# Optimization experiments

Hardware: AMD Instinct MI355X
Metric: run time of the kernel (lower is better)

## Reference

```python
import jax, jax.numpy as jnp
import numpy as np
import math

FEAT_DIM = 128
N_BANK = 1000000
K_NEG = 4096
BATCH = 256
T = 0.5
MOMENTUM = 0.5
EPS = 1e-7


def setup_inputs() -> dict:
    key = jax.random.key(0)
    k1, k2, k3, k4, k5, k6 = jax.random.split(key, 6)
    stdv = 1.0 / math.sqrt(FEAT_DIM / 3)
    memory_l = jax.random.uniform(k1, (N_BANK, FEAT_DIM), minval=-stdv, maxval=stdv, dtype=jnp.float32)
    memory_ab = jax.random.uniform(k2, (N_BANK, FEAT_DIM), minval=-stdv, maxval=stdv, dtype=jnp.float32)
    l = jax.random.normal(k3, (BATCH, FEAT_DIM), dtype=jnp.float32)
    ab = jax.random.normal(k4, (BATCH, FEAT_DIM), dtype=jnp.float32)
    y = jax.random.randint(k5, (BATCH,), 0, N_BANK, dtype=jnp.int32)
    idx = jax.random.randint(k6, (BATCH, K_NEG + 1), 0, N_BANK, dtype=jnp.int32)
    idx = idx.at[:, 0].set(y)  # positive sample in slot 0, as in torch forward
    return {"l": l, "ab": ab, "memory_l": memory_l, "memory_ab": memory_ab, "y": y, "idx": idx}


def _l2_normalize(x):
    # matches torch: x / (sqrt(sum(x^2)) + eps)
    return x / (jnp.sqrt(jnp.sum(x * x, axis=1, keepdims=True)) + EPS)


def _momentum_update(memory, y, x_norm):
    # gather rows, momentum mix, renormalize, scatter back
    pos = memory[y] * MOMENTUM + x_norm * (1.0 - MOMENTUM)          # [B, D]
    norm = jnp.sqrt(jnp.sum(pos * pos, axis=1, keepdims=True))
    return memory.at[y].set(pos / norm)


def reference(l, ab, memory_l, memory_ab, y, idx):
    outputSize = memory_l.shape[0]
    ln = _l2_normalize(l)
    abn = _l2_normalize(ab)

    # gather negatives+positive from the AB bank, score against l features
    w_ab = jax.lax.stop_gradient(memory_ab[idx])                     # [B, K+1, D]
    P_l = jnp.exp(jnp.einsum('bkd,bd->bk', w_ab, ln) / T)[..., None]  # [B, K+1, 1]
    Z_l = jnp.mean(P_l) * outputSize
    out_l = P_l / Z_l

    w_l = jax.lax.stop_gradient(memory_l[idx])                       # [B, K+1, D]
    P_ab = jnp.exp(jnp.einsum('bkd,bd->bk', w_l, abn) / T)[..., None]
    Z_ab = jnp.mean(P_ab) * outputSize
    out_ab = P_ab / Z_ab

    # momentum scatter update of the memory banks (no_grad in torch)
    new_memory_l = jax.lax.stop_gradient(_momentum_update(memory_l, y, ln))
    new_memory_ab = jax.lax.stop_gradient(_momentum_update(memory_ab, y, abn))

    return out_l, out_ab, new_memory_l, new_memory_ab
```

## Files before the change

### kernel.cpp

```cpp
#include <hip/hip_runtime.h>
#include <math.h>
#include <stdint.h>

#define FEAT   128
#define NBANK  1000000
#define KP1    4097
#define BATCH  256
#define INV_T  2.0f
#define EPS_N  1e-7f

constexpr size_t TOTP   = (size_t)BATCH * KP1;
constexpr size_t O_OUTL = 0;
constexpr size_t O_OUTA = TOTP;
constexpr size_t O_MEML = 2 * TOTP;
constexpr size_t O_MEMA = O_MEML + (size_t)NBANK * FEAT;

constexpr int RPB   = 16;
constexpr int NBUCK = NBANK / RPB;
constexpr int CAP   = 128;

constexpr size_t WS_LN   = 0;
constexpr size_t WS_ABN  = 32768;
constexpr size_t WS_PL   = 65544;
constexpr size_t WS_PA   = 65800;
constexpr size_t WS_U32  = 66560;

typedef float vfloat4 __attribute__((ext_vector_type(4)));

__device__ __forceinline__ float dot4(vfloat4 a, vfloat4 b) {
    return a.x * b.x + a.y * b.y + a.z * b.z + a.w * b.w;
}

__global__ void norm_zero_kernel(const float* __restrict__ l,
                                 const float* __restrict__ ab,
                                 float* __restrict__ ws,
                                 unsigned int* __restrict__ cnt) {
    int b    = blockIdx.x;
    int lane = threadIdx.x;
    for (int i = b * 64 + lane; i < NBUCK; i += 512 * 64) cnt[i] = 0u;
    const float* src;
    float*       dst;
    if (b < BATCH) { src = l  + (size_t)b * FEAT;            dst = ws + WS_LN  + (size_t)b * FEAT; }
    else           { src = ab + (size_t)(b - BATCH) * FEAT;  dst = ws + WS_ABN + (size_t)(b - BATCH) * FEAT; }
    float2 v = *(const float2*)(src + 2 * lane);
    float  ss = v.x * v.x + v.y * v.y;
    #pragma unroll
    for (int m = 1; m < 64; m <<= 1) ss += __shfl_xor(ss, m, 64);
    float inv = 1.0f / (sqrtf(ss) + EPS_N);
    ((float2*)dst)[lane] = make_float2(v.x * inv, v.y * inv);
}

__global__ void build_kernel(const int* __restrict__ idx,
                             unsigned int* __restrict__ cnt,
                             unsigned int* __restrict__ ent) {
    size_t stride = (size_t)gridDim.x * blockDim.x;
    for (size_t p = (size_t)blockIdx.x * blockDim.x + threadIdx.x; p < TOTP; p += stride) {
        int row = idx[p];
        int b   = (int)(p / KP1);
        int k   = (int)(p - (size_t)b * KP1);
        int bucket = row >> 4;
        unsigned int pos = atomicAdd(&cnt[bucket], 1u);
        if (pos < (unsigned int)CAP)
            ent[(size_t)bucket * CAP + pos] =
                ((unsigned int)b << 17) | ((unsigned int)k << 4) | (unsigned int)(row & 15);
    }
}

__global__ __launch_bounds__(256) void copyscore_kernel(
        const float* __restrict__ src, float* __restrict__ dst,
        const float* __restrict__ qtab, float* __restrict__ pout,
        const unsigned int* __restrict__ cnt,
        const unsigned int* __restrict__ ent) {
    int blk = blockIdx.x;
    int tid = threadIdx.x;
    size_t fbase = (size_t)blk * RPB * FEAT;

    int c = min((int)cnt[blk], CAP);

    const vfloat4* s = (const vfloat4*)(src + fbase);
    vfloat4 v0 = s[tid], v1 = s[256 + tid];
    vfloat4* d = (vfloat4*)(dst + fbase);
    d[tid] = v0; d[256 + tid] = v1;

    int g = tid >> 4, lane16 = tid & 15;
    for (int i = g; i < c; i += 16) {
        unsigned int ev = ent[(size_t)blk * CAP + i];
        int rloc = (int)(ev & 15u);
        int k    = (int)((ev >> 4) & 0x1FFFu);
        int b    = (int)(ev >> 17);
        const vfloat4* rp = (const vfloat4*)(src + fbase + (size_t)rloc * FEAT) + lane16 * 2;
        vfloat4 w0 = rp[0], w1 = rp[1];
        const vfloat4* qp = (const vfloat4*)(qtab + (size_t)b * FEAT) + lane16 * 2;
        vfloat4 q0 = qp[0], q1 = qp[1];
        float dv = dot4(w0, q0) + dot4(w1, q1);
        #pragma unroll
        for (int m = 1; m < 16; m <<= 1) dv += __shfl_xor(dv, m, 64);
        if (lane16 == 0) pout[(size_t)b * KP1 + k] = __expf(dv * INV_T);
    }
}

__global__ void zsum_kernel(const float* __restrict__ out,
                            float* __restrict__ pl, float* __restrict__ pa) {
    __shared__ float sl[256], sa[256];
    int i = blockIdx.x, t = threadIdx.x;
    const float* bl = out + O_OUTL + (size_t)i * KP1;
    const float* ba = out + O_OUTA + (size_t)i * KP1;
    float a = 0.f, b = 0.f;
    for (int p = t; p < KP1; p += 256) { a += bl[p]; b += ba[p]; }
    sl[t] = a; sa[t] = b;
    __syncthreads();
    for (int s = 128; s > 0; s >>= 1) {
        if (t < s) { sl[t] += sl[t + s]; sa[t] += sa[t + s]; }
        __syncthreads();
    }
    if (t == 0) { pl[i] = sl[0]; pa[i] = sa[0]; }
}

__global__ void finish_kernel(const float* __restrict__ pl,
                              const float* __restrict__ pa,
                              const float* __restrict__ mem_l,
                              const float* __restrict__ mem_ab,
                              const int*   __restrict__ y,
                              const float* __restrict__ ws,
                              float* __restrict__ out) {
    __shared__ float s2[2];
    int b = blockIdx.x, t = threadIdx.x;
    if (t == 0) {
        float a = 0.f, c = 0.f;
        for (int i = 0; i < 256; ++i) { a += pl[i]; c += pa[i]; }
        float count = (float)TOTP;
        s2[0] = count / (a * (float)NBANK);
        s2[1] = count / (c * (float)NBANK);
    }
    __syncthreads();
    float zl = s2[0], za = s2[1];
    float* bl = out + O_OUTL + (size_t)b * KP1;
    float* ba = out + O_OUTA + (size_t)b * KP1;
    for (int p = t; p < KP1; p += 256) { bl[p] *= zl; ba[p] *= za; }

    if (t < 64) {
        int lane = t;
        int row  = y[b];
        bool win = true;
        for (int j = b + 1; j < BATCH; ++j)
            if (y[j] == row) { win = false; break; }
        if (win) {
            {
                float2 m = ((const float2*)(mem_l + (size_t)row * FEAT))[lane];
                float2 x = ((const float2*)(ws + WS_LN + (size_t)b * FEAT))[lane];
                float2 p = make_float2(m.x * 0.5f + x.x * 0.5f, m.y * 0.5f + x.y * 0.5f);
                float ss = p.x * p.x + p.y * p.y;
                #pragma unroll
                for (int mk = 1; mk < 64; mk <<= 1) ss += __shfl_xor(ss, mk, 64);
                float nrm = sqrtf(ss);
                ((float2*)(out + O_MEML + (size_t)row * FEAT))[lane] =
                    make_float2(p.x / nrm, p.y / nrm);
            }
            {
                float2 m = ((const float2*)(mem_ab + (size_t)row * FEAT))[lane];
                float2 x = ((const float2*)(ws + WS_ABN + (size_t)b * FEAT))[lane];
                float2 p = make_float2(m.x * 0.5f + x.x * 0.5f, m.y * 0.5f + x.y * 0.5f);
                float ss = p.x * p.x + p.y * p.y;
                #pragma unroll
                for (int mk = 1; mk < 64; mk <<= 1) ss += __shfl_xor(ss, mk, 64);
                float nrm = sqrtf(ss);
                ((float2*)(out + O_MEMA + (size_t)row * FEAT))[lane] =
                    make_float2(p.x / nrm, p.y / nrm);
            }
        }
    }
}

extern "C" void kernel_launch(void* const* d_in, const int* in_sizes, int n_in,
                              void* d_out, int out_size, void* d_ws, size_t ws_size,
                              hipStream_t stream) {
    const float* l      = (const float*)d_in[0];
    const float* ab     = (const float*)d_in[1];
    const float* mem_l  = (const float*)d_in[2];
    const float* mem_ab = (const float*)d_in[3];
    const int*   y      = (const int*)d_in[4];
    const int*   idx    = (const int*)d_in[5];
    float* out = (float*)d_out;
    float* ws  = (float*)d_ws;

    unsigned int* wsu = (unsigned int*)(ws + WS_U32);
    unsigned int* cnt = wsu;
    unsigned int* ent = wsu + NBUCK;

    norm_zero_kernel<<<dim3(2 * BATCH), dim3(64), 0, stream>>>(l, ab, ws, cnt);
    build_kernel<<<dim3(2048), dim3(256), 0, stream>>>(idx, cnt, ent);
    copyscore_kernel<<<dim3(NBUCK), dim3(256), 0, stream>>>(
        mem_l, out + O_MEML, ws + WS_ABN, out + O_OUTA, cnt, ent);
    copyscore_kernel<<<dim3(NBUCK), dim3(256), 0, stream>>>(
        mem_ab, out + O_MEMA, ws + WS_LN, out + O_OUTL, cnt, ent);
    zsum_kernel<<<dim3(256), dim3(256), 0, stream>>>(out, ws + WS_PL, ws + WS_PA);
    finish_kernel<<<dim3(BATCH), dim3(256), 0, stream>>>(
        ws + WS_PL, ws + WS_PA, mem_l, mem_ab, y, ws, out);
}
```

Baseline: 515.7 us.

## Fuse both bank copy-score passes into one persistent kernel with LDS staging and prefetch

```diff
diff --git a/kernel.cpp b/kernel.cpp
--- a/kernel.cpp
+++ b/kernel.cpp
@@ -17,7 +17,10 @@
 
 constexpr int RPB   = 16;
 constexpr int NBUCK = NBANK / RPB;
-constexpr int CAP   = 128;
+constexpr int CAP   = 64;
+
+constexpr int CHUNK  = 31;
+constexpr int GRID_M = (NBUCK + CHUNK - 1) / CHUNK;
 
 constexpr size_t WS_LN   = 0;
 constexpr size_t WS_ABN  = 32768;
@@ -66,36 +69,76 @@
     }
 }
 
-__global__ __launch_bounds__(256) void copyscore_kernel(
-        const float* __restrict__ src, float* __restrict__ dst,
-        const float* __restrict__ qtab, float* __restrict__ pout,
+__global__ __launch_bounds__(256) void main_kernel(
+        const float* __restrict__ mem_l, const float* __restrict__ mem_ab,
+        const float* __restrict__ ws_f,
         const unsigned int* __restrict__ cnt,
-        const unsigned int* __restrict__ ent) {
-    int blk = blockIdx.x;
+        const unsigned int* __restrict__ ent,
+        float* __restrict__ out) {
+    __shared__ float ldsL[RPB * FEAT];
+    __shared__ float ldsA[RPB * FEAT];
     int tid = threadIdx.x;
-    size_t fbase = (size_t)blk * RPB * FEAT;
-
-    int c = min((int)cnt[blk], CAP);
-
-    const vfloat4* s = (const vfloat4*)(src + fbase);
-    vfloat4 v0 = s[tid], v1 = s[256 + tid];
-    vfloat4* d = (vfloat4*)(dst + fbase);
-    d[tid] = v0; d[256 + tid] = v1;
-
+    int w0  = blockIdx.x * CHUNK;
+    int w1  = min(w0 + CHUNK, NBUCK);
+    if (w0 >= NBUCK) return;
+
+    vfloat4* lL = (vfloat4*)ldsL;
+    vfloat4* lA = (vfloat4*)ldsA;
     int g = tid >> 4, lane16 = tid & 15;
-    for (int i = g; i < c; i += 16) {
-        unsigned int ev = ent[(size_t)blk * CAP + i];
-        int rloc = (int)(ev & 15u);
-        int k    = (int)((ev >> 4) & 0x1FFFu);
-        int b    = (int)(ev >> 17);
-        const vfloat4* rp = (const vfloat4*)(src + fbase + (size_t)rloc * FEAT) + lane16 * 2;
-        vfloat4 w0 = rp[0], w1 = rp[1];
-        const vfloat4* qp = (const vfloat4*)(qtab + (size_t)b * FEAT) + lane16 * 2;
-        vfloat4 q0 = qp[0], q1 = qp[1];
-        float dv = dot4(w0, q0) + dot4(w1, q1);
-        #pragma unroll
-        for (int m = 1; m < 16; m <<= 1) dv += __shfl_xor(dv, m, 64);
-        if (lane16 == 0) pout[(size_t)b * KP1 + k] = __expf(dv * INV_T);
+
+    size_t fb = (size_t)w0 * RPB * FEAT;
+    vfloat4 cl0 = ((const vfloat4*)(mem_l  + fb))[tid];
+    vfloat4 cl1 = ((const vfloat4*)(mem_l  + fb))[256 + tid];
+    vfloat4 ca0 = ((const vfloat4*)(mem_ab + fb))[tid];
+    vfloat4 ca1 = ((const vfloat4*)(mem_ab + fb))[256 + tid];
+    int c = min((int)cnt[w0], CAP);
+
+    for (int w = w0; w < w1; ++w) {
+        size_t fbase = (size_t)w * RPB * FEAT;
+        lL[tid] = cl0; lL[256 + tid] = cl1;
+        lA[tid] = ca0; lA[256 + tid] = ca1;
+        ((vfloat4*)(out + O_MEML + fbase))[tid]       = cl0;
+        ((vfloat4*)(out + O_MEML + fbase))[256 + tid] = cl1;
+        ((vfloat4*)(out + O_MEMA + fbase))[tid]       = ca0;
+        ((vfloat4*)(out + O_MEMA + fbase))[256 + tid] = ca1;
+        vfloat4 nl0, nl1, na0, na1; int cn = 0;
+        if (w + 1 < w1) {
+            size_t nb = (size_t)(w + 1) * RPB * FEAT;
+            nl0 = ((const vfloat4*)(mem_l  + nb))[tid];
+            nl1 = ((const vfloat4*)(mem_l  + nb))[256 + tid];
+            na0 = ((const vfloat4*)(mem_ab + nb))[tid];
+            na1 = ((const vfloat4*)(mem_ab + nb))[256 + tid];
+            cn  = min((int)cnt[w + 1], CAP);
+        }
+        asm volatile("s_waitcnt lgkmcnt(0)" ::: "memory");
+        __builtin_amdgcn_s_barrier();
+        for (int i = g; i < c; i += 16) {
+            unsigned int ev = ent[(size_t)w * CAP + i];
+            int rloc = (int)(ev & 15u);
+            int k    = (int)((ev >> 4) & 0x1FFFu);
+            int b    = (int)(ev >> 17);
+            const vfloat4* ra = (const vfloat4*)(ldsA + rloc * FEAT) + lane16 * 2;
+            const vfloat4* rl = (const vfloat4*)(ldsL + rloc * FEAT) + lane16 * 2;
+            vfloat4 wa0 = ra[0], wa1 = ra[1];
+            vfloat4 wl0 = rl[0], wl1 = rl[1];
+            const vfloat4* lq = (const vfloat4*)(ws_f + WS_LN  + (size_t)b * FEAT) + lane16 * 2;
+            const vfloat4* aq = (const vfloat4*)(ws_f + WS_ABN + (size_t)b * FEAT) + lane16 * 2;
+            vfloat4 lv0 = lq[0], lv1 = lq[1];
+            vfloat4 av0 = aq[0], av1 = aq[1];
+            float dlv  = dot4(wa0, lv0) + dot4(wa1, lv1);
+            float dabv = dot4(wl0, av0) + dot4(wl1, av1);
+            #pragma unroll
+            for (int m = 1; m < 16; m <<= 1) {
+                dlv  += __shfl_xor(dlv,  m, 64);
+                dabv += __shfl_xor(dabv, m, 64);
+            }
+            if (lane16 == 0) {
+                out[O_OUTL + (size_t)b * KP1 + k] = __expf(dlv  * INV_T);
+                out[O_OUTA + (size_t)b * KP1 + k] = __expf(dabv * INV_T);
+            }
+        }
+        __builtin_amdgcn_s_barrier();
+        cl0 = nl0; cl1 = nl1; ca0 = na0; ca1 = na1; c = cn;
     }
 }
 
@@ -189,10 +232,8 @@
 
     norm_zero_kernel<<<dim3(2 * BATCH), dim3(64), 0, stream>>>(l, ab, ws, cnt);
     build_kernel<<<dim3(2048), dim3(256), 0, stream>>>(idx, cnt, ent);
-    copyscore_kernel<<<dim3(NBUCK), dim3(256), 0, stream>>>(
-        mem_l, out + O_MEML, ws + WS_ABN, out + O_OUTA, cnt, ent);
-    copyscore_kernel<<<dim3(NBUCK), dim3(256), 0, stream>>>(
-        mem_ab, out + O_MEMA, ws + WS_LN, out + O_OUTL, cnt, ent);
+    main_kernel<<<dim3(GRID_M), dim3(256), 0, stream>>>(
+        mem_l, mem_ab, ws, cnt, ent, out);
     zsum_kernel<<<dim3(256), dim3(256), 0, stream>>>(out, ws + WS_PL, ws + WS_PA);
     finish_kernel<<<dim3(BATCH), dim3(256), 0, stream>>>(
         ws + WS_PL, ws + WS_PA, mem_l, mem_ab, y, ws, out);
```

Result: slower. 573.3 us (+11.2%).
